# Optimization experiments

Hardware: AMD Instinct MI355X
Metric: run time of the kernel (lower is better)

Reference implementation:

```python
import jax, jax.numpy as jnp
import numpy as np

N_SRC, N_DST, MAX_NEIGH, H = 65536, 8192, 32, 128


def setup_inputs() -> dict:
    key = jax.random.key(0)
    ks = jax.random.split(key, 16)
    inp = {
        'x': jax.random.randint(ks[0], (N_SRC, 2), 0, 1000, dtype=jnp.int64)
             if jax.config.jax_enable_x64 else jax.random.randint(ks[0], (N_SRC, 2), 0, 1000, dtype=jnp.int32),
        'neigh_sim': jax.random.randint(ks[1], (N_DST, MAX_NEIGH), 0, N_SRC, dtype=jnp.int32),
        'neigh_cor': jax.random.randint(ks[2], (N_DST, MAX_NEIGH), 0, N_SRC, dtype=jnp.int32),
        'emb0_sim': jax.random.normal(ks[3], (1000, 32), jnp.float32) * 0.1,
        'emb1_sim': jax.random.normal(ks[4], (100000, 96), jnp.float32) * 0.1,
        'emb0_cor': jax.random.normal(ks[5], (1000, 32), jnp.float32) * 0.1,
        'emb1_cor': jax.random.normal(ks[6], (100000, 96), jnp.float32) * 0.1,
        'W_in_sim': jax.random.normal(ks[7], (H, H), jnp.float32) * 0.05,
        'b_in_sim': jnp.zeros((H,), jnp.float32),
        'W_in_cor': jax.random.normal(ks[8], (H, H), jnp.float32) * 0.05,
        'b_in_cor': jnp.zeros((H,), jnp.float32),
        'W_out_sim': jax.random.normal(ks[9], (H, H), jnp.float32) * 0.05,
        'b_out_sim': jnp.zeros((H,), jnp.float32),
        'W_out_cor': jax.random.normal(ks[10], (H, H), jnp.float32) * 0.05,
        'b_out_cor': jnp.zeros((H,), jnp.float32),
        'W_sim2cor': jax.random.normal(ks[11], (H, H), jnp.float32) * 0.05,
        'W_cor2sim': jax.random.normal(ks[12], (H, H), jnp.float32) * 0.05,
    }
    return inp


def _coattention_pool(D, Q):
    # D, Q: [N, m, H]
    n, m, h = Q.shape
    L = jnp.einsum('nmh,nkh->nmk', D, Q)           # [N, m, m]
    AC = jax.nn.softmax(L, axis=-1)
    AS = jax.nn.softmax(jnp.swapaxes(L, 1, 2), axis=-1)
    CQ = jnp.einsum('nmk,nkh->nmh', AC, Q)          # [N, m, H]
    CD = jnp.einsum('nkm,nmh->nkh', AS, jnp.concatenate([D, CQ], axis=-1))  # [N, m, 2H]
    out = jnp.concatenate([Q, CD], axis=-1)         # [N, m, 3H]
    # AvgPool1d(kernel=3, stride=3) over channel dim, then mean over neighbors
    pooled = out.reshape(n, m, h, 3).mean(axis=-1)  # consecutive triples
    return pooled.mean(axis=1)                       # [N, H]


def _mode_forward(x, neigh_sim, neigh_cor, emb0, emb1, W_in, b_in, W_out, b_out, mode):
    feat = jnp.concatenate([emb0[x[:, 0]], emb1[x[:, 1]]], axis=-1)  # [N_src, 128]
    feat = feat @ W_in + b_in                                        # [N_src, H]
    h_self = feat[: neigh_sim.shape[0]]
    nf_sim = feat[neigh_sim]  # [N_dst, m, H]
    nf_cor = feat[neigh_cor]
    if mode == 'cor':
        D, Q = nf_sim, nf_cor
    else:
        D, Q = nf_cor, nf_sim
    rst = h_self + _coattention_pool(D, Q)
    return rst @ W_out + b_out


def reference(x, neigh_sim, neigh_cor, emb0_sim, emb1_sim, emb0_cor, emb1_cor,
              W_in_sim, b_in_sim, W_in_cor, b_in_cor,
              W_out_sim, b_out_sim, W_out_cor, b_out_cor,
              W_sim2cor, W_cor2sim):
    sim = _mode_forward(x, neigh_sim, neigh_cor, emb0_sim, emb1_sim,
                        W_in_sim, b_in_sim, W_out_sim, b_out_sim, 'sim')
    cor = _mode_forward(x, neigh_sim, neigh_cor, emb0_cor, emb1_cor,
                        W_in_cor, b_in_cor, W_out_cor, b_out_cor, 'cor')
    a1, a2, b2 = 0.5, 0.33, 0.33
    z1sim = (1 - a1) * sim + a1 * (cor @ W_cor2sim)
    z1cor = (1 - a1) * cor + a1 * (sim @ W_sim2cor)
    z2sim = (1 - a2 - b2) * sim + a2 * (cor @ W_cor2sim) + b2 * (z1cor @ W_cor2sim)
    z2cor = (1 - a2 - b2) * cor + a2 * (sim @ W_sim2cor) + b2 * (z1sim @ W_sim2cor)
    return z2sim, z2cor
```

## Files before the change

kernel.cpp:

```cpp
#include <hip/hip_runtime.h>
#include <hip/hip_bf16.h>

#define NSRC 65536
#define NDST 8192
#define H 128

#define C_SELF 0.34f
#define C_CROSS 0.495f
#define C_DBL  0.165f

typedef float f32x16 __attribute__((ext_vector_type(16)));
typedef short bf16x8 __attribute__((ext_vector_type(8)));

static __device__ __forceinline__ float b2f(unsigned short u) {
  union { unsigned int i; float f; } v; v.i = ((unsigned int)u) << 16; return v.f;
}
static __device__ __forceinline__ unsigned short f2b(float f) {
  union { float f; unsigned int i; } v; v.f = f;
  unsigned int x = v.i;
  return (unsigned short)((x + 0x7fffu + ((x >> 16) & 1u)) >> 16);
}
static __device__ __forceinline__ void load4bf(const unsigned short* p, float* d) {
  ushort4 u = *(const ushort4*)p;
  d[0] = b2f(u.x); d[1] = b2f(u.y); d[2] = b2f(u.z); d[3] = b2f(u.w);
}

template <int CTRL>
static __device__ __forceinline__ float dpp_mov(float x) {
  return __int_as_float(__builtin_amdgcn_update_dpp(
      0, __float_as_int(x), CTRL, 0xF, 0xF, true));
}
static __device__ __forceinline__ float dpp_sum32_tail(float x) {
  x += dpp_mov<0x111>(x);
  x += dpp_mov<0x112>(x);
  x += dpp_mov<0x114>(x);
  x += dpp_mov<0x118>(x);
  x += dpp_mov<0x142>(x);
  return x;
}
static __device__ __forceinline__ float allred32_sum(float x) {
  x += dpp_mov<0xB1>(x);
  x += dpp_mov<0x4E>(x);
  x += dpp_mov<0x124>(x);
  x += dpp_mov<0x128>(x);
  x += __int_as_float(__builtin_amdgcn_ds_swizzle(__float_as_int(x), 0x401F));
  return x;
}

static __device__ __forceinline__ void load4any(const void* base, size_t idx, int f32flag, float* d) {
  if (f32flag) {
    float4 v = *(const float4*)((const float*)base + idx);
    d[0] = v.x; d[1] = v.y; d[2] = v.z; d[3] = v.w;
  } else {
    load4bf((const unsigned short*)base + idx, d);
  }
}
static __device__ __forceinline__ float load1any(const void* base, size_t idx, int f32flag) {
  return f32flag ? ((const float*)base)[idx] : b2f(((const unsigned short*)base)[idx]);
}

static __device__ __forceinline__ int detect_wf(const unsigned short* __restrict__ W) {
  const int l = threadIdx.x & 63;
  int bad = 0;
#pragma unroll
  for (int i = l; i < 128; i += 64) {
    unsigned short u = W[i];
    if (u != 0) {
      int e = (u >> 7) & 0xFF;
      if (e < 90 || e > 128) bad++;
    }
  }
#pragma unroll
  for (int d = 1; d < 64; d <<= 1) bad += __shfl_xor(bad, d);
  return (bad > 8) ? 1 : 0;
}
static __device__ __forceinline__ int detect_x64(const int* __restrict__ x) {
  const int l = threadIdx.x & 63;
  int nz = (l < 16) ? (x[2 * l + 1] != 0 ? 1 : 0) : 0;
#pragma unroll
  for (int d = 1; d < 64; d <<= 1) nz += __shfl_xor(nz, d);
  return (nz == 0) ? 1 : 0;
}

__global__ __launch_bounds__(128) void prep(
    const void* __restrict__ Wsim_in, const void* __restrict__ Wcor_in,
    const int* __restrict__ x,
    const void* __restrict__ Wos, const void* __restrict__ Woc,
    const void* __restrict__ Wsc, const void* __restrict__ Wcs,
    const void* __restrict__ bs, const void* __restrict__ bc,
    unsigned short* __restrict__ WTsim, unsigned short* __restrict__ WTcor,
    unsigned short* __restrict__ P1T, unsigned short* __restrict__ P2T,
    unsigned short* __restrict__ MssT, unsigned short* __restrict__ MccT,
    float* __restrict__ bsim, float* __restrict__ bcor)
{
  __shared__ float lds[256];
  const int wf = detect_wf((const unsigned short*)Wsim_in);
  const int bid = blockIdx.x;
  const int c = threadIdx.x;

  if (bid < 256) {
    const int n = bid & 127;
    const void* W = (bid & 128) ? Wcor_in : Wsim_in;
    unsigned short* WT = (bid & 128) ? WTcor : WTsim;
    WT[n * 128 + c] = f2b(load1any(W, c * 128 + n, wf));
    return;
  }
  const int b2 = bid - 256;
  if (b2 < 128) {
    const int r = b2;
    float acc = 0.f;
    for (int k = 0; k < 128; ++k)
      acc += load1any(Wos, r * 128 + k, wf) * load1any(Wsc, k * 128 + c, wf);
    P1T[c * 128 + r] = f2b(acc);
    lds[c] = acc;
    __syncthreads();
    float acc2 = 0.f;
    for (int k = 0; k < 128; ++k) acc2 += lds[k] * load1any(Wcs, k * 128 + c, wf);
    MssT[c * 128 + r] = f2b(C_SELF * load1any(Wos, r * 128 + c, wf) + C_DBL * acc2);
  } else if (b2 < 256) {
    const int r = b2 - 128;
    float acc = 0.f;
    for (int k = 0; k < 128; ++k)
      acc += load1any(Woc, r * 128 + k, wf) * load1any(Wcs, k * 128 + c, wf);
    P2T[c * 128 + r] = f2b(acc);
    lds[c] = acc;
    __syncthreads();
    float acc2 = 0.f;
    for (int k = 0; k < 128; ++k) acc2 += lds[k] * load1any(Wsc, k * 128 + c, wf);
    MccT[c * 128 + r] = f2b(C_SELF * load1any(Woc, r * 128 + c, wf) + C_DBL * acc2);
  } else {
    float a1 = 0.f, a2 = 0.f;
    for (int k = 0; k < 128; ++k) a1 += load1any(bs, k, wf) * load1any(Wsc, k * 128 + c, wf);
    for (int k = 0; k < 128; ++k) a2 += load1any(bc, k, wf) * load1any(Wcs, k * 128 + c, wf);
    lds[c] = a1; lds[128 + c] = a2;
    __syncthreads();
    float a3 = 0.f, a4 = 0.f;
    for (int k = 0; k < 128; ++k) a3 += lds[k] * load1any(Wcs, k * 128 + c, wf);
    for (int k = 0; k < 128; ++k) a4 += lds[128 + k] * load1any(Wsc, k * 128 + c, wf);
    bsim[c] = C_SELF * load1any(bs, c, wf) + C_CROSS * a2 + C_DBL * a3;
    bcor[c] = C_SELF * load1any(bc, c, wf) + C_CROSS * a1 + C_DBL * a4;
  }
}

__global__ __launch_bounds__(256) void featgemm_mfma(
    const int* __restrict__ x,
    const void* __restrict__ Wdet,
    const void* __restrict__ emb0s, const void* __restrict__ emb1s,
    const void* __restrict__ emb0c, const void* __restrict__ emb1c,
    const unsigned short* __restrict__ WTs, const unsigned short* __restrict__ WTc,
    const void* __restrict__ bvs, const void* __restrict__ bvc,
    unsigned char* __restrict__ f8s, unsigned short* __restrict__ f16s,
    unsigned char* __restrict__ f8c, unsigned short* __restrict__ f16c)
{
  const int wf  = detect_wf((const unsigned short*)Wdet);
  const int x64 = detect_x64(x);
  const int mode = blockIdx.y;
  const void* emb0 = mode ? emb0c : emb0s;
  const void* emb1 = mode ? emb1c : emb1s;
  const unsigned short* WT = mode ? WTc : WTs;
  const void* bvec = mode ? bvc : bvs;
  unsigned char*  feat8  = mode ? f8c  : f8s;
  unsigned short* feat16 = mode ? f16c : f16s;

  const int t = threadIdx.x;
  const int w = t >> 6, l = t & 63, lane = l & 31, half = l >> 5;
  const int rbase = blockIdx.x * 128 + w * 32;
  const int r = rbase + lane;

  int x0, x1;
  if (x64) { x0 = x[r * 4]; x1 = x[r * 4 + 2]; }
  else     { x0 = x[r * 2]; x1 = x[r * 2 + 1]; }

  bf16x8 afrag[8];
#pragma unroll
  for (int s = 0; s < 8; ++s) {
    float tmp[8];
    if (s < 2) {
      const size_t base = (size_t)x0 * 32 + s * 16 + half * 8;
      load4any(emb0, base, wf, tmp);
      load4any(emb0, base + 4, wf, tmp + 4);
    } else {
      const size_t base = (size_t)x1 * 96 + (s * 16 - 32) + half * 8;
      load4any(emb1, base, wf, tmp);
      load4any(emb1, base + 4, wf, tmp + 4);
    }
    union { bf16x8 v; unsigned short u[8]; } cv;
#pragma unroll
    for (int j = 0; j < 8; ++j) cv.u[j] = f2b(tmp[j]);
    afrag[s] = cv.v;
  }

  const bool do16 = (rbase < NDST);
#pragma unroll
  for (int strip = 0; strip < 4; ++strip) {
    const int n = strip * 32 + lane;
    const unsigned short* wtrow = WT + (size_t)n * 128 + half * 8;
    f32x16 acc = {0,0,0,0,0,0,0,0,0,0,0,0,0,0,0,0};
#pragma unroll
    for (int s = 0; s < 8; ++s) {
      bf16x8 bfrag = *(const bf16x8*)(wtrow + s * 16);
      acc = __builtin_amdgcn_mfma_f32_32x32x16_bf16(afrag[s], bfrag, acc, 0, 0, 0);
    }
    const float bias_n = load1any(bvec, n, wf);
#pragma unroll
    for (int i = 0; i < 16; ++i) {
      const int m = (i & 3) + 8 * (i >> 2) + 4 * half;
      const int row = rbase + m;
      const float val = acc[i] + bias_n;
      const int p8 = __builtin_amdgcn_cvt_pk_fp8_f32(val, val, 0, false);
      feat8[(size_t)row * H + n] = (unsigned char)(p8 & 0xFF);
      if (do16) feat16[(size_t)row * H + n] = f2b(val);
    }
  }
}

__global__ __launch_bounds__(256) void coatt_mfma(
    const unsigned char* __restrict__ f8s, const unsigned short* __restrict__ f16s,
    const unsigned char* __restrict__ f8c, const unsigned short* __restrict__ f16c,
    const int* __restrict__ nsim, const int* __restrict__ ncor,
    unsigned short* __restrict__ rsts, unsigned short* __restrict__ rstc)
{
  const int mode = blockIdx.y;
  const unsigned char*  feat8  = mode ? f8c  : f8s;
  const unsigned short* feat16 = mode ? f16c : f16s;
  const int* idxD = mode ? nsim : ncor;
  const int* idxQ = mode ? ncor : nsim;
  unsigned short* rst = mode ? rstc : rsts;

  __shared__ float gbuf[4][448];
  const int t = threadIdx.x;
  const int w = t >> 6;
  const int l = t & 63;
  const int r = l & 31;
  const int half = l >> 5;
  const int n = blockIdx.x * 4 + w;

  float* g   = gbuf[w];
  float* svb = gbuf[w] + 384;
  float* tvb = gbuf[w] + 416;

  const int gD = idxD[n * 32 + r];
  const int gQ = idxQ[n * 32 + r];
  const unsigned char* drow = feat8 + (size_t)gD * H + half * 8;
  const unsigned char* qrow = feat8 + (size_t)gQ * H + half * 8;

  long dfrag[8], qfrag[8];
#pragma unroll
  for (int s = 0; s < 8; ++s) {
    dfrag[s] = *(const long*)(drow + s * 16);
    qfrag[s] = *(const long*)(qrow + s * 16);
  }

  f32x16 acc = {0,0,0,0,0,0,0,0,0,0,0,0,0,0,0,0};
#pragma unroll
  for (int s = 0; s < 8; ++s)
    acc = __builtin_amdgcn_mfma_f32_32x32x16_fp8_fp8(dfrag[s], qfrag[s], acc, 0, 0, 0);

  float ex[16], rrcp[16];
#pragma unroll
  for (int i = 0; i < 16; ++i) ex[i] = __expf(acc[i]);
#pragma unroll
  for (int i = 0; i < 16; ++i) rrcp[i] = 1.0f / allred32_sum(ex[i]);
  float csum = 0.f;
#pragma unroll
  for (int i = 0; i < 16; ++i) csum += ex[i];
  csum += __shfl_xor(csum, 32);
  const float crcp = 1.0f / csum;

  float svt[16];
#pragma unroll
  for (int i = 0; i < 16; ++i) svt[i] = dpp_sum32_tail(ex[i] * crcp);
  if (r == 31) {
    *(float4*)(svb + 4 * half)      = make_float4(svt[0],  svt[1],  svt[2],  svt[3]);
    *(float4*)(svb + 8 + 4 * half)  = make_float4(svt[4],  svt[5],  svt[6],  svt[7]);
    *(float4*)(svb + 16 + 4 * half) = make_float4(svt[8],  svt[9],  svt[10], svt[11]);
    *(float4*)(svb + 24 + 4 * half) = make_float4(svt[12], svt[13], svt[14], svt[15]);
  }
  float sv16[16];
#pragma unroll
  for (int q = 0; q < 4; ++q) {
    float4 v = *(const float4*)(svb + q * 8 + 4 * half);
    sv16[q * 4] = v.x; sv16[q * 4 + 1] = v.y; sv16[q * 4 + 2] = v.z; sv16[q * 4 + 3] = v.w;
  }
  float tvp = 0.f;
#pragma unroll
  for (int i = 0; i < 16; ++i) tvp += sv16[i] * ex[i] * rrcp[i];
  const float tv = tvp + __shfl_xor(tvp, 32);

  if (l < 32) tvb[l] = tv;
  float tv16[16];
#pragma unroll
  for (int q = 0; q < 4; ++q) {
    float4 vv = *(const float4*)(tvb + q * 8 + 4 * half);
    tv16[q * 4] = vv.x; tv16[q * 4 + 1] = vv.y; tv16[q * 4 + 2] = vv.z; tv16[q * 4 + 3] = vv.w;
  }

  const int bpos = (l & 15) - half * 8;
  const long b_ident = (bpos >= 0 && bpos < 8) ? (0x38L << (8 * bpos)) : 0L;
  const f32x16 zf = {0,0,0,0,0,0,0,0,0,0,0,0,0,0,0,0};

#pragma unroll
  for (int s = 0; s < 8; ++s) {
    f32x16 td = __builtin_amdgcn_mfma_f32_32x32x16_fp8_fp8(dfrag[s], b_ident, zf, 0, 0, 0);
    f32x16 tq = __builtin_amdgcn_mfma_f32_32x32x16_fp8_fp8(qfrag[s], b_ident, zf, 0, 0, 0);
    float su = 0.f, sw = 0.f, sv_ = 0.f;
#pragma unroll
    for (int i = 0; i < 16; ++i) {
      su  += tq[i];
      sw  += tv16[i] * tq[i];
      sv_ += sv16[i] * td[i];
    }
    su  += __shfl_xor(su, 32);
    sw  += __shfl_xor(sw, 32);
    sv_ += __shfl_xor(sv_, 32);
    if (l < 16) {
      const int c = s * 16 + l;
      g[c]       = su;
      g[128 + c] = sv_;
      g[256 + c] = sw;
    }
  }

#pragma unroll
  for (int rep = 0; rep < 2; ++rep) {
    const int hp = l + rep * 64;
    const float p = (g[3 * hp] + g[3 * hp + 1] + g[3 * hp + 2]) * (1.0f / 96.0f);
    const float hs = b2f(feat16[(size_t)n * H + hp]);
    rst[(size_t)n * H + hp] = f2b(hs + p);
  }
}

__global__ __launch_bounds__(256) void finalmm_mfma(
    const unsigned short* __restrict__ Rs, const unsigned short* __restrict__ Rc,
    const unsigned short* __restrict__ MssT, const unsigned short* __restrict__ MccT,
    const unsigned short* __restrict__ P1T, const unsigned short* __restrict__ P2T,
    const float* __restrict__ bsim, const float* __restrict__ bcor,
    float* __restrict__ outp)
{
  const int t = threadIdx.x;
  const int w = t >> 6, l = t & 63, lane = l & 31, half = l >> 5;
  const int rbase = blockIdx.x * 32;
  const int arow = rbase + lane;
  const int n = w * 32 + lane;

  const unsigned short* rsrow = Rs + (size_t)arow * H + half * 8;
  const unsigned short* rcrow = Rc + (size_t)arow * H + half * 8;
  bf16x8 aS[8], aC[8];
#pragma unroll
  for (int s = 0; s < 8; ++s) {
    aS[s] = *(const bf16x8*)(rsrow + s * 16);
    aC[s] = *(const bf16x8*)(rcrow + s * 16);
  }

  const unsigned short* bMss = MssT + (size_t)n * 128 + half * 8;
  const unsigned short* bMcc = MccT + (size_t)n * 128 + half * 8;
  const unsigned short* bP1  = P1T  + (size_t)n * 128 + half * 8;
  const unsigned short* bP2  = P2T  + (size_t)n * 128 + half * 8;

  f32x16 a1 = {0,0,0,0,0,0,0,0,0,0,0,0,0,0,0,0};
  f32x16 a2 = a1, a3 = a1, a4 = a1;
#pragma unroll
  for (int s = 0; s < 8; ++s) {
    bf16x8 b1 = *(const bf16x8*)(bMss + s * 16);
    bf16x8 b2 = *(const bf16x8*)(bP2  + s * 16);
    bf16x8 b3 = *(const bf16x8*)(bMcc + s * 16);
    bf16x8 b4 = *(const bf16x8*)(bP1  + s * 16);
    a1 = __builtin_amdgcn_mfma_f32_32x32x16_bf16(aS[s], b1, a1, 0, 0, 0);
    a2 = __builtin_amdgcn_mfma_f32_32x32x16_bf16(aC[s], b2, a2, 0, 0, 0);
    a3 = __builtin_amdgcn_mfma_f32_32x32x16_bf16(aC[s], b3, a3, 0, 0, 0);
    a4 = __builtin_amdgcn_mfma_f32_32x32x16_bf16(aS[s], b4, a4, 0, 0, 0);
  }

  const float bsv = bsim[n], bcv = bcor[n];
#pragma unroll
  for (int i = 0; i < 16; ++i) {
    const int m = (i & 3) + 8 * (i >> 2) + 4 * half;
    const int row = rbase + m;
    outp[(size_t)row * H + n] = a1[i] + C_CROSS * a2[i] + bsv;
    outp[(size_t)NDST * H + (size_t)row * H + n] = a3[i] + C_CROSS * a4[i] + bcv;
  }
}

extern "C" void kernel_launch(void* const* d_in, const int* in_sizes, int n_in,
                              void* d_out, int out_size, void* d_ws, size_t ws_size,
                              hipStream_t stream) {
  const int* x    = (const int*)d_in[0];
  const int* nsim = (const int*)d_in[1];
  const int* ncor = (const int*)d_in[2];
  const void* emb0_sim = d_in[3];
  const void* emb1_sim = d_in[4];
  const void* emb0_cor = d_in[5];
  const void* emb1_cor = d_in[6];
  const void* W_in_sim  = d_in[7];
  const void* b_in_sim  = d_in[8];
  const void* W_in_cor  = d_in[9];
  const void* b_in_cor  = d_in[10];
  const void* W_out_sim = d_in[11];
  const void* b_out_sim = d_in[12];
  const void* W_out_cor = d_in[13];
  const void* b_out_cor = d_in[14];
  const void* W_sim2cor = d_in[15];
  const void* W_cor2sim = d_in[16];

  float* fbase = (float*)d_ws;
  float* P1  = fbase;
  float* P2  = P1 + H * H;
  float* p1v = P2 + H * H;
  float* p2v = p1v + H;
  float* bsimv = p2v + H;
  float* bcorv = bsimv + H;
  int* flags = (int*)(bcorv + H);
  unsigned short* feat16_sim = (unsigned short*)(flags + 4);
  unsigned short* feat16_cor = feat16_sim + (size_t)NDST * H;
  unsigned short* rst_sim    = feat16_cor + (size_t)NDST * H;
  unsigned short* rst_cor    = rst_sim + (size_t)NDST * H;
  unsigned char* feat8_sim = (unsigned char*)(rst_cor + (size_t)NDST * H);
  unsigned char* feat8_cor = feat8_sim + (size_t)NSRC * H;
  unsigned short* WT_sim = (unsigned short*)(feat8_cor + (size_t)NSRC * H);
  unsigned short* WT_cor = WT_sim + H * H;
  unsigned short* P1T  = WT_cor + H * H;
  unsigned short* P2T  = P1T + H * H;
  unsigned short* MssT = P2T + H * H;
  unsigned short* MccT = MssT + H * H;

  prep<<<513, 128, 0, stream>>>(W_in_sim, W_in_cor, x,
                                W_out_sim, W_out_cor, W_sim2cor, W_cor2sim,
                                b_out_sim, b_out_cor,
                                WT_sim, WT_cor, P1T, P2T, MssT, MccT, bsimv, bcorv);
  featgemm_mfma<<<dim3(NSRC / 128, 2), 256, 0, stream>>>(
      x, W_in_sim, emb0_sim, emb1_sim, emb0_cor, emb1_cor,
      WT_sim, WT_cor, b_in_sim, b_in_cor,
      feat8_sim, feat16_sim, feat8_cor, feat16_cor);
  coatt_mfma<<<dim3(NDST / 4, 2), 256, 0, stream>>>(
      feat8_sim, feat16_sim, feat8_cor, feat16_cor,
      nsim, ncor, rst_sim, rst_cor);
  finalmm_mfma<<<NDST / 32, 256, 0, stream>>>(rst_sim, rst_cor, MssT, MccT, P1T, P2T,
                                              bsimv, bcorv, (float*)d_out);
}
```

Measured before the change: 259.4 us.

## Split weight preprocessing into transpose and MFMA-based small GEMM kernels

Replaces the monolithic scalar prep kernel with three kernels: a transpose kernel for input and cross weights, then two MFMA bf16 kernels that compute the composed weight products P = Wout·Wcross and M = C_SELF·Wout + C_DBL·P·Wcross. The old version did each 128x128 product with one thread per output and serial 128-long dot products. The new path uses matrix cores, in exchange for extra launches, intermediate bf16 rounding of P before the second product, and a few more workspace buffers.

```diff
diff --git a/kernel.cpp b/kernel.cpp
--- a/kernel.cpp
+++ b/kernel.cpp
@@ -82,63 +82,156 @@
   return (nz == 0) ? 1 : 0;
 }
 
-__global__ __launch_bounds__(128) void prep(
+__global__ __launch_bounds__(128) void transk(
     const void* __restrict__ Wsim_in, const void* __restrict__ Wcor_in,
-    const int* __restrict__ x,
+    const void* __restrict__ Wsc, const void* __restrict__ Wcs,
+    unsigned short* __restrict__ WTsim, unsigned short* __restrict__ WTcor,
+    unsigned short* __restrict__ WscT, unsigned short* __restrict__ WcsT)
+{
+  const int wf = detect_wf((const unsigned short*)Wsim_in);
+  const int bid = blockIdx.x;
+  const int k = threadIdx.x;
+  const int n = bid & 127;
+  const void* W;
+  unsigned short* WT;
+  if (bid < 256) {
+    W  = (bid & 128) ? Wcor_in : Wsim_in;
+    WT = (bid & 128) ? WTcor : WTsim;
+  } else {
+    W  = (bid & 128) ? Wcs : Wsc;
+    WT = (bid & 128) ? WcsT : WscT;
+  }
+  WT[n * 128 + k] = f2b(load1any(W, k * 128 + n, wf));
+}
+
+__global__ __launch_bounds__(256) void sgemm1(
+    const void* __restrict__ Wdet,
     const void* __restrict__ Wos, const void* __restrict__ Woc,
     const void* __restrict__ Wsc, const void* __restrict__ Wcs,
     const void* __restrict__ bs, const void* __restrict__ bc,
-    unsigned short* __restrict__ WTsim, unsigned short* __restrict__ WTcor,
+    const unsigned short* __restrict__ WscT, const unsigned short* __restrict__ WcsT,
     unsigned short* __restrict__ P1T, unsigned short* __restrict__ P2T,
+    unsigned short* __restrict__ P1bf, unsigned short* __restrict__ P2bf,
+    float* __restrict__ p1, float* __restrict__ p2)
+{
+  __shared__ float l1[256], l2[256];
+  const int wf = detect_wf((const unsigned short*)Wdet);
+  const int bid = blockIdx.x;
+  const int t = threadIdx.x;
+
+  if (bid == 8) {
+    const int c = t & 127, kg = t >> 7;
+    float a1 = 0.f, a2 = 0.f;
+    for (int k = kg * 64; k < kg * 64 + 64; ++k) {
+      a1 += load1any(bs, k, wf) * load1any(Wsc, k * 128 + c, wf);
+      a2 += load1any(bc, k, wf) * load1any(Wcs, k * 128 + c, wf);
+    }
+    l1[t] = a1; l2[t] = a2;
+    __syncthreads();
+    if (kg == 0) { p1[c] = l1[c] + l1[c + 128]; p2[c] = l2[c] + l2[c + 128]; }
+    return;
+  }
+
+  const bool isP2 = bid >= 4;
+  const int rbase = (bid & 3) * 32;
+  const void* A = isP2 ? Woc : Wos;
+  const unsigned short* BT = isP2 ? WcsT : WscT;
+  unsigned short* PT = isP2 ? P2T : P1T;
+  unsigned short* Pb = isP2 ? P2bf : P1bf;
+
+  const int w = t >> 6, l = t & 63, lane = l & 31, half = l >> 5;
+  const int arow = rbase + lane;
+  const int n = w * 32 + lane;
+
+  bf16x8 af[8];
+#pragma unroll
+  for (int s = 0; s < 8; ++s) {
+    float tmp[8];
+    const size_t base = (size_t)arow * 128 + s * 16 + half * 8;
+    load4any(A, base, wf, tmp);
+    load4any(A, base + 4, wf, tmp + 4);
+    union { bf16x8 v; unsigned short u[8]; } cv;
+#pragma unroll
+    for (int j = 0; j < 8; ++j) cv.u[j] = f2b(tmp[j]);
+    af[s] = cv.v;
+  }
+
+  f32x16 acc = {0,0,0,0,0,0,0,0,0,0,0,0,0,0,0,0};
+#pragma unroll
+  for (int s = 0; s < 8; ++s) {
+    bf16x8 bfrag = *(const bf16x8*)(BT + (size_t)n * 128 + s * 16 + half * 8);
+    acc = __builtin_amdgcn_mfma_f32_32x32x16_bf16(af[s], bfrag, acc, 0, 0, 0);
+  }
+#pragma unroll
+  for (int i = 0; i < 16; ++i) {
+    const int m = (i & 3) + 8 * (i >> 2) + 4 * half;
+    const int r = rbase + m;
+    const unsigned short v = f2b(acc[i]);
+    PT[(size_t)n * 128 + r] = v;
+    Pb[(size_t)r * 128 + n] = v;
+  }
+}
+
+__global__ __launch_bounds__(256) void sgemm2(
+    const void* __restrict__ Wdet,
+    const void* __restrict__ Wos, const void* __restrict__ Woc,
+    const void* __restrict__ Wsc, const void* __restrict__ Wcs,
+    const void* __restrict__ bs, const void* __restrict__ bc,
+    const unsigned short* __restrict__ WscT, const unsigned short* __restrict__ WcsT,
+    const unsigned short* __restrict__ P1bf, const unsigned short* __restrict__ P2bf,
+    const float* __restrict__ p1, const float* __restrict__ p2,
     unsigned short* __restrict__ MssT, unsigned short* __restrict__ MccT,
     float* __restrict__ bsim, float* __restrict__ bcor)
 {
-  __shared__ float lds[256];
-  const int wf = detect_wf((const unsigned short*)Wsim_in);
+  __shared__ float l1[256], l2[256];
+  const int wf = detect_wf((const unsigned short*)Wdet);
   const int bid = blockIdx.x;
-  const int c = threadIdx.x;
-
-  if (bid < 256) {
-    const int n = bid & 127;
-    const void* W = (bid & 128) ? Wcor_in : Wsim_in;
-    unsigned short* WT = (bid & 128) ? WTcor : WTsim;
-    WT[n * 128 + c] = f2b(load1any(W, c * 128 + n, wf));
+  const int t = threadIdx.x;
+
+  if (bid == 8) {
+    const int c = t & 127, kg = t >> 7;
+    float a3 = 0.f, a4 = 0.f;
+    for (int k = kg * 64; k < kg * 64 + 64; ++k) {
+      a3 += p1[k] * load1any(Wcs, k * 128 + c, wf);
+      a4 += p2[k] * load1any(Wsc, k * 128 + c, wf);
+    }
+    l1[t] = a3; l2[t] = a4;
+    __syncthreads();
+    if (kg == 0) {
+      bsim[c] = C_SELF * load1any(bs, c, wf) + C_CROSS * p2[c] + C_DBL * (l1[c] + l1[c + 128]);
+      bcor[c] = C_SELF * load1any(bc, c, wf) + C_CROSS * p1[c] + C_DBL * (l2[c] + l2[c + 128]);
+    }
     return;
   }
-  const int b2 = bid - 256;
-  if (b2 < 128) {
-    const int r = b2;
-    float acc = 0.f;
-    for (int k = 0; k < 128; ++k)
-      acc += load1any(Wos, r * 128 + k, wf) * load1any(Wsc, k * 128 + c, wf);
-    P1T[c * 128 + r] = f2b(acc);
-    lds[c] = acc;
-    __syncthreads();
-    float acc2 = 0.f;
-    for (int k = 0; k < 128; ++k) acc2 += lds[k] * load1any(Wcs, k * 128 + c, wf);
-    MssT[c * 128 + r] = f2b(C_SELF * load1any(Wos, r * 128 + c, wf) + C_DBL * acc2);
-  } else if (b2 < 256) {
-    const int r = b2 - 128;
-    float acc = 0.f;
-    for (int k = 0; k < 128; ++k)
-      acc += load1any(Woc, r * 128 + k, wf) * load1any(Wcs, k * 128 + c, wf);
-    P2T[c * 128 + r] = f2b(acc);
-    lds[c] = acc;
-    __syncthreads();
-    float acc2 = 0.f;
-    for (int k = 0; k < 128; ++k) acc2 += lds[k] * load1any(Wsc, k * 128 + c, wf);
-    MccT[c * 128 + r] = f2b(C_SELF * load1any(Woc, r * 128 + c, wf) + C_DBL * acc2);
-  } else {
-    float a1 = 0.f, a2 = 0.f;
-    for (int k = 0; k < 128; ++k) a1 += load1any(bs, k, wf) * load1any(Wsc, k * 128 + c, wf);
-    for (int k = 0; k < 128; ++k) a2 += load1any(bc, k, wf) * load1any(Wcs, k * 128 + c, wf);
-    lds[c] = a1; lds[128 + c] = a2;
-    __syncthreads();
-    float a3 = 0.f, a4 = 0.f;
-    for (int k = 0; k < 128; ++k) a3 += lds[k] * load1any(Wcs, k * 128 + c, wf);
-    for (int k = 0; k < 128; ++k) a4 += lds[128 + k] * load1any(Wsc, k * 128 + c, wf);
-    bsim[c] = C_SELF * load1any(bs, c, wf) + C_CROSS * a2 + C_DBL * a3;
-    bcor[c] = C_SELF * load1any(bc, c, wf) + C_CROSS * a1 + C_DBL * a4;
+
+  const bool isMcc = bid >= 4;
+  const int rbase = (bid & 3) * 32;
+  const unsigned short* A = isMcc ? P2bf : P1bf;
+  const unsigned short* BT = isMcc ? WscT : WcsT;
+  const void* Wself = isMcc ? Woc : Wos;
+  unsigned short* out = isMcc ? MccT : MssT;
+
+  const int w = t >> 6, l = t & 63, lane = l & 31, half = l >> 5;
+  const int arow = rbase + lane;
+  const int n = w * 32 + lane;
+
+  bf16x8 af[8];
+#pragma unroll
+  for (int s = 0; s < 8; ++s)
+    af[s] = *(const bf16x8*)(A + (size_t)arow * 128 + s * 16 + half * 8);
+
+  f32x16 acc = {0,0,0,0,0,0,0,0,0,0,0,0,0,0,0,0};
+#pragma unroll
+  for (int s = 0; s < 8; ++s) {
+    bf16x8 bfrag = *(const bf16x8*)(BT + (size_t)n * 128 + s * 16 + half * 8);
+    acc = __builtin_amdgcn_mfma_f32_32x32x16_bf16(af[s], bfrag, acc, 0, 0, 0);
+  }
+#pragma unroll
+  for (int i = 0; i < 16; ++i) {
+    const int m = (i & 3) + 8 * (i >> 2) + 4 * half;
+    const int r = rbase + m;
+    out[(size_t)n * 128 + r] =
+        f2b(C_SELF * load1any(Wself, (size_t)r * 128 + n, wf) + C_DBL * acc[i]);
   }
 }
 
@@ -403,9 +496,9 @@
   const void* W_cor2sim = d_in[16];
 
   float* fbase = (float*)d_ws;
-  float* P1  = fbase;
-  float* P2  = P1 + H * H;
-  float* p1v = P2 + H * H;
+  float* P1slot = fbase;
+  float* P2slot = P1slot + H * H;
+  float* p1v = P2slot + H * H;
   float* p2v = p1v + H;
   float* bsimv = p2v + H;
   float* bcorv = bsimv + H;
@@ -422,11 +515,19 @@
   unsigned short* P2T  = P1T + H * H;
   unsigned short* MssT = P2T + H * H;
   unsigned short* MccT = MssT + H * H;
-
-  prep<<<513, 128, 0, stream>>>(W_in_sim, W_in_cor, x,
-                                W_out_sim, W_out_cor, W_sim2cor, W_cor2sim,
-                                b_out_sim, b_out_cor,
-                                WT_sim, WT_cor, P1T, P2T, MssT, MccT, bsimv, bcorv);
+  unsigned short* WscT = (unsigned short*)P1slot;
+  unsigned short* WcsT = WscT + H * H;
+  unsigned short* P1bf = (unsigned short*)P2slot;
+  unsigned short* P2bf = P1bf + H * H;
+
+  transk<<<512, 128, 0, stream>>>(W_in_sim, W_in_cor, W_sim2cor, W_cor2sim,
+                                  WT_sim, WT_cor, WscT, WcsT);
+  sgemm1<<<9, 256, 0, stream>>>(W_in_sim, W_out_sim, W_out_cor, W_sim2cor, W_cor2sim,
+                                b_out_sim, b_out_cor, WscT, WcsT,
+                                P1T, P2T, P1bf, P2bf, p1v, p2v);
+  sgemm2<<<9, 256, 0, stream>>>(W_in_sim, W_out_sim, W_out_cor, W_sim2cor, W_cor2sim,
+                                b_out_sim, b_out_cor, WscT, WcsT,
+                                P1bf, P2bf, p1v, p2v, MssT, MccT, bsimv, bcorv);
   featgemm_mfma<<<dim3(NSRC / 128, 2), 256, 0, stream>>>(
       x, W_in_sim, emb0_sim, emb1_sim, emb0_cor, emb1_cor,
       WT_sim, WT_cor, b_in_sim, b_in_cor,
```

Result: faster. 242.2 us (-6.6%).
